# Optimization experiments

Hardware: AMD Instinct MI355X
Metric: run time of the kernel (lower is better)

The kernel has to match this reference:

```python
import jax, jax.numpy as jnp
import numpy as np

def setup_inputs() -> dict:
    key = jax.random.key(0)
    k1, k2, k3 = jax.random.split(key, 3)
    N, C, H, W = 16, 128, 128, 128
    out_chn = 128
    x = jax.random.normal(k1, (N, C, H, W), dtype=jnp.float32)
    # 1x1 conv = per-pixel linear: weight (out_chn, in_chn), bias (out_chn,)
    fan_in = C  # kernel_size=1 -> fan_in = in_chn
    bound = 1.0 / np.sqrt(fan_in)
    conv_w = jax.random.uniform(k2, (out_chn, C), dtype=jnp.float32, minval=-bound, maxval=bound)
    conv_b = jax.random.uniform(k3, (out_chn,), dtype=jnp.float32, minval=-bound, maxval=bound)
    return {"x": x, "conv_w": conv_w, "conv_b": conv_b}

def reference(x, conv_w, conv_b):
    N, C, H, W = x.shape
    x_hw = x.reshape(N, C, H * W)                     # (N, C, HW)
    logits = jnp.einsum('ncl,ndl->ncd', x_hw, x_hw)    # (N, C, C), unscaled
    weights = jax.nn.softmax(logits, axis=-1)
    attn = jnp.einsum('ncd,ndl->ncl', weights, x_hw)   # (N, C, HW)
    attn = attn.reshape(N, C, H, W)
    # 1x1 conv: contract over channel dim
    out = jnp.einsum('nchw,oc->nohw', attn, conv_w) + conv_b[None, :, None, None]
    return out
```

## Files before the change

### kernel.cpp

```cpp
#include <hip/hip_runtime.h>
#include <hip/hip_bf16.h>
#include <stdint.h>

#define NB    16
#define CD    128
#define HW    16384
#define KSPLIT 32

typedef float  f32x4  __attribute__((ext_vector_type(4)));
typedef short  bf16x8 __attribute__((ext_vector_type(8)));

__device__ __forceinline__ unsigned f2bf(float f) {
    unsigned u = __float_as_uint(f);
    u += 0x7FFFu + ((u >> 16) & 1u);
    return u >> 16;
}

__device__ __forceinline__ unsigned pk2bf(float a, float b) {
    return f2bf(a) | (f2bf(b) << 16);
}

__global__ __launch_bounds__(256, 2) void gram_kernel(const float* __restrict__ x,
                                                      float* __restrict__ P) {
    const int n  = blockIdx.x;
    const int kc = blockIdx.y;
    const int t    = threadIdx.x;
    const int wv   = t >> 6;
    const int lane = t & 63;
    const int q    = lane >> 4;
    const int r16  = lane & 15;

    __shared__ __align__(16) unsigned short Xl[CD * 132];

    f32x4 acc[4][4];
#pragma unroll
    for (int i = 0; i < 4; ++i)
#pragma unroll
        for (int j = 0; j < 4; ++j) acc[i][j] = (f32x4)0.0f;

    const int rt0 = 4 * (wv >> 1);
    const int ct0 = 4 * (wv & 1);

    const float* xb = x + (size_t)n * CD * HW;

    const int cS = t >> 5;
    const int lS = (t & 31) * 4;

    float4 stg[16];
#pragma unroll
    for (int i = 0; i < 16; ++i)
        stg[i] = *(const float4*)(xb + (size_t)(i * 8 + cS) * HW + kc * 512 + lS);

    for (int sub = 0; sub < 4; ++sub) {
#pragma unroll
        for (int i = 0; i < 16; ++i) {
            uint2 pk;
            pk.x = pk2bf(stg[i].x, stg[i].y);
            pk.y = pk2bf(stg[i].z, stg[i].w);
            *(uint2*)(&Xl[(i * 8 + cS) * 132 + lS]) = pk;
        }
        __syncthreads();

        if (sub < 3) {
            const int kb = kc * 512 + (sub + 1) * 128;
#pragma unroll
            for (int i = 0; i < 16; ++i)
                stg[i] = *(const float4*)(xb + (size_t)(i * 8 + cS) * HW + kb + lS);
        }

#pragma unroll
        for (int ks = 0; ks < 4; ++ks) {
            const int k0 = ks * 32 + q * 8;
            bf16x8 af[4], bfr[4];
#pragma unroll
            for (int i = 0; i < 4; ++i) {
                const unsigned short* pa = &Xl[(16 * (rt0 + i) + r16) * 132 + k0];
                union { bf16x8 v; uint2 u[2]; } ua;
                ua.u[0] = *(const uint2*)pa;
                ua.u[1] = *(const uint2*)(pa + 4);
                af[i] = ua.v;
                const unsigned short* pb = &Xl[(16 * (ct0 + i) + r16) * 132 + k0];
                union { bf16x8 v; uint2 u[2]; } ub;
                ub.u[0] = *(const uint2*)pb;
                ub.u[1] = *(const uint2*)(pb + 4);
                bfr[i] = ub.v;
            }
#pragma unroll
            for (int i = 0; i < 4; ++i)
#pragma unroll
                for (int j = 0; j < 4; ++j)
                    acc[i][j] = __builtin_amdgcn_mfma_f32_16x16x32_bf16(
                        af[i], bfr[j], acc[i][j], 0, 0, 0);
        }
        __syncthreads();
    }

    float* Pn = P + ((size_t)kc * NB + n) * CD * CD;
#pragma unroll
    for (int i = 0; i < 4; ++i)
#pragma unroll
        for (int j = 0; j < 4; ++j)
#pragma unroll
            for (int rr = 0; rr < 4; ++rr) {
                int row = 16 * (rt0 + i) + q * 4 + rr;
                int col = 16 * (ct0 + j) + r16;
                Pn[row * CD + col] = acc[i][j][rr];
            }
}

__global__ __launch_bounds__(256) void reduce_kernel(const float* __restrict__ P,
                                                     float* __restrict__ E) {
    const int R    = blockIdx.x * 4 + (threadIdx.x >> 6);
    const int lane = threadIdx.x & 63;
    const int n    = R >> 7;
    const int row  = R & 127;

    const float* p = P + (size_t)n * CD * CD + (size_t)row * CD;
    float s0 = 0.0f, s1 = 0.0f;
#pragma unroll
    for (int kc = 0; kc < KSPLIT; ++kc) {
        const float* pk = p + (size_t)kc * NB * CD * CD;
        s0 += pk[lane];
        s1 += pk[lane + 64];
    }
    float m = fmaxf(s0, s1);
#pragma unroll
    for (int off = 32; off > 0; off >>= 1) m = fmaxf(m, __shfl_xor(m, off));
    const float e0 = __expf(s0 - m);
    const float e1 = __expf(s1 - m);
    float e = e0 + e1;
#pragma unroll
    for (int off = 32; off > 0; off >>= 1) e += __shfl_xor(e, off);
    const float inv = 1.0f / e;

    float* g = E + (size_t)n * CD * CD + (size_t)row * CD;
    g[lane]      = e0 * inv;
    g[lane + 64] = e1 * inv;
}

__global__ __launch_bounds__(256) void mmat_kernel(const float* __restrict__ E,
                                                   const float* __restrict__ cw,
                                                   unsigned short* __restrict__ Mbf) {
    const int n  = blockIdx.x;
    const int bo = blockIdx.y;
    const int t  = threadIdx.x;
    const int o  = bo * 8 + (t >> 5);
    const int d0 = (t & 31) * 4;

    const float* En  = E + (size_t)n * CD * CD;
    const float* cwo = cw + (size_t)o * CD;

    float a0 = 0, a1 = 0, a2 = 0, a3 = 0;
#pragma unroll 8
    for (int c = 0; c < CD; ++c) {
        const float cv = cwo[c];
        float4 w = *(const float4*)&En[c * CD + d0];
        a0 += cv * w.x; a1 += cv * w.y; a2 += cv * w.z; a3 += cv * w.w;
    }
    uint2 pk;
    pk.x = pk2bf(a0, a1);
    pk.y = pk2bf(a2, a3);
    *(uint2*)&Mbf[((size_t)n * CD + o) * CD + d0] = pk;
}

__global__ __launch_bounds__(256) void out_kernel(const float* __restrict__ x,
                                                  const unsigned short* __restrict__ Mbf,
                                                  const float* __restrict__ bias,
                                                  float* __restrict__ out) {
    const int lb = blockIdx.x;
    const int n  = blockIdx.y;
    const int l0 = lb * 128;
    const int t    = threadIdx.x;
    const int wv   = t >> 6;
    const int lane = t & 63;
    const int q    = lane >> 4;
    const int r16  = lane & 15;

    __shared__ __align__(16) unsigned short Xt[128 * 128];
    __shared__ float bl[CD];

    const int lt0 = 4 * (wv >> 1);
    const int ot0 = 4 * (wv & 1);

    if (t < CD) bl[t] = bias[t];

    const float* xb = x + (size_t)n * CD * HW + l0;
    const int lt = t & 31;
    const int dg = t >> 5;
#pragma unroll
    for (int i = 0; i < 4; ++i) {
        const int d0 = i * 32 + dg * 4;
        const float* bp = xb + (size_t)d0 * HW + 4 * lt;
        float4 v0 = *(const float4*)(bp);
        float4 v1 = *(const float4*)(bp + HW);
        float4 v2 = *(const float4*)(bp + 2 * HW);
        float4 v3 = *(const float4*)(bp + 3 * HW);
        float r0[4] = {v0.x, v0.y, v0.z, v0.w};
        float r1[4] = {v1.x, v1.y, v1.z, v1.w};
        float r2[4] = {v2.x, v2.y, v2.z, v2.w};
        float r3[4] = {v3.x, v3.y, v3.z, v3.w};
        const int dph = d0 ^ (8 * (lt & 7));
#pragma unroll
        for (int j = 0; j < 4; ++j) {
            uint2 pk;
            pk.x = pk2bf(r0[j], r1[j]);
            pk.y = pk2bf(r2[j], r3[j]);
            *(uint2*)&Xt[(4 * lt + j) * 128 + dph] = pk;
        }
    }
    __syncthreads();

    f32x4 acc[4][4];
#pragma unroll
    for (int i = 0; i < 4; ++i)
#pragma unroll
        for (int j = 0; j < 4; ++j) acc[i][j] = (f32x4)0.0f;

    const unsigned short* Mn = Mbf + (size_t)n * CD * CD;
#pragma unroll
    for (int ks = 0; ks < 4; ++ks) {
        const int k0 = ks * 32 + q * 8;
        bf16x8 bfr[4];
#pragma unroll
        for (int j = 0; j < 4; ++j) {
            const int o = 16 * (ot0 + j) + r16;
            union { bf16x8 v; uint4 u; } ub;
            ub.u = *(const uint4*)&Mn[o * CD + k0];
            bfr[j] = ub.v;
        }
        bf16x8 af[4];
#pragma unroll
        for (int i = 0; i < 4; ++i) {
            const int l = 16 * (lt0 + i) + r16;
            const int doff = k0 ^ (8 * ((l >> 2) & 7));
            union { bf16x8 v; uint4 u; } ua;
            ua.u = *(const uint4*)&Xt[l * 128 + doff];
            af[i] = ua.v;
        }
#pragma unroll
        for (int i = 0; i < 4; ++i)
#pragma unroll
            for (int j = 0; j < 4; ++j)
                acc[i][j] = __builtin_amdgcn_mfma_f32_16x16x32_bf16(
                    af[i], bfr[j], acc[i][j], 0, 0, 0);
    }

    float* ob = out + (size_t)n * CD * HW + l0;
#pragma unroll
    for (int i = 0; i < 4; ++i)
#pragma unroll
        for (int j = 0; j < 4; ++j) {
            const int o = 16 * (ot0 + j) + r16;
            const int l = 16 * (lt0 + i) + q * 4;
            const float b = bl[o];
            float4 st;
            st.x = acc[i][j][0] + b;
            st.y = acc[i][j][1] + b;
            st.z = acc[i][j][2] + b;
            st.w = acc[i][j][3] + b;
            *(float4*)(ob + (size_t)o * HW + l) = st;
        }
}

extern "C" void kernel_launch(void* const* d_in, const int* in_sizes, int n_in,
                              void* d_out, int out_size, void* d_ws, size_t ws_size,
                              hipStream_t stream) {
    const float* x  = (const float*)d_in[0];
    const float* cw = (const float*)d_in[1];
    const float* cb = (const float*)d_in[2];
    float* out = (float*)d_out;

    char* ws = (char*)d_ws;
    float*          P   = (float*)(ws);
    float*          E   = (float*)(ws + (32u << 20));
    unsigned short* Mbf = (unsigned short*)(ws + (33u << 20));

    gram_kernel   <<<dim3(NB, KSPLIT), 256, 0, stream>>>(x, P);
    reduce_kernel <<<dim3(512),        256, 0, stream>>>(P, E);
    mmat_kernel   <<<dim3(NB, 16),     256, 0, stream>>>(E, cw, Mbf);
    out_kernel    <<<dim3(128, NB),    256, 0, stream>>>(x, Mbf, cb, out);
}
```

Baseline: 303.4 us.

## Fuse four stages into one cooperative kernel with grid syncs

Replaces the four separate launches (gram, reduce/softmax, weight-mix matrix, output GEMM) with a single cooperative kernel of 512 blocks that separates the stages with grid-wide syncs, keeping the separate launches as a fallback. The aim is to remove launch gaps and per-kernel tail effects between dependent stages. The reduce step also switches to float2 loads and stores. The costs are three grid barriers and a fixed 512-block grid for the output stage, where each block now loops over 4 tiles instead of one tile per block. The fused kernel needs 512 blocks to be co-resident, otherwise the cooperative launch fails and the old path runs.

Result: slower. 634.0 us (+109.0%).

```diff
diff --git a/kernel.cpp b/kernel.cpp
--- a/kernel.cpp
+++ b/kernel.cpp
@@ -1,6 +1,8 @@
 #include <hip/hip_runtime.h>
-#include <hip/hip_bf16.h>
+#include <hip/hip_cooperative_groups.h>
 #include <stdint.h>
+
+namespace cg = cooperative_groups;
 
 #define NB    16
 #define CD    128
@@ -15,9 +17,241 @@
     u += 0x7FFFu + ((u >> 16) & 1u);
     return u >> 16;
 }
-
 __device__ __forceinline__ unsigned pk2bf(float a, float b) {
     return f2bf(a) | (f2bf(b) << 16);
+}
+
+__global__ __launch_bounds__(256, 2) void fused_kernel(
+    const float* __restrict__ x, const float* __restrict__ cw,
+    const float* __restrict__ cb, float* __restrict__ P,
+    float* __restrict__ E, unsigned short* __restrict__ Mbf,
+    float* __restrict__ out)
+{
+    const int b    = blockIdx.x;
+    const int t    = threadIdx.x;
+    const int wv   = t >> 6;
+    const int lane = t & 63;
+    const int q    = lane >> 4;
+    const int r16  = lane & 15;
+
+    __shared__ __align__(16) unsigned short sh[CD * 132];
+    float* bl = (float*)(sh + CD * 128);
+
+    {
+        const int n  = b >> 5;
+        const int kc = b & 31;
+        unsigned short* Xl = sh;
+
+        f32x4 acc[4][4];
+#pragma unroll
+        for (int i = 0; i < 4; ++i)
+#pragma unroll
+            for (int j = 0; j < 4; ++j) acc[i][j] = (f32x4)0.0f;
+
+        const int rt0 = 4 * (wv >> 1);
+        const int ct0 = 4 * (wv & 1);
+        const float* xb = x + (size_t)n * CD * HW;
+        const int cS = t >> 5;
+        const int lS = (t & 31) * 4;
+
+        float4 stg[16];
+#pragma unroll
+        for (int i = 0; i < 16; ++i)
+            stg[i] = *(const float4*)(xb + (size_t)(i * 8 + cS) * HW + kc * 512 + lS);
+
+        for (int sub = 0; sub < 4; ++sub) {
+#pragma unroll
+            for (int i = 0; i < 16; ++i) {
+                uint2 pk;
+                pk.x = pk2bf(stg[i].x, stg[i].y);
+                pk.y = pk2bf(stg[i].z, stg[i].w);
+                *(uint2*)(&Xl[(i * 8 + cS) * 132 + lS]) = pk;
+            }
+            __syncthreads();
+
+            if (sub < 3) {
+                const int kb = kc * 512 + (sub + 1) * 128;
+#pragma unroll
+                for (int i = 0; i < 16; ++i)
+                    stg[i] = *(const float4*)(xb + (size_t)(i * 8 + cS) * HW + kb + lS);
+            }
+
+#pragma unroll
+            for (int ks = 0; ks < 4; ++ks) {
+                const int k0 = ks * 32 + q * 8;
+                bf16x8 af[4], bfr[4];
+#pragma unroll
+                for (int i = 0; i < 4; ++i) {
+                    const unsigned short* pa = &Xl[(16 * (rt0 + i) + r16) * 132 + k0];
+                    union { bf16x8 v; uint2 u[2]; } ua;
+                    ua.u[0] = *(const uint2*)pa;
+                    ua.u[1] = *(const uint2*)(pa + 4);
+                    af[i] = ua.v;
+                    const unsigned short* pb = &Xl[(16 * (ct0 + i) + r16) * 132 + k0];
+                    union { bf16x8 v; uint2 u[2]; } ub;
+                    ub.u[0] = *(const uint2*)pb;
+                    ub.u[1] = *(const uint2*)(pb + 4);
+                    bfr[i] = ub.v;
+                }
+#pragma unroll
+                for (int i = 0; i < 4; ++i)
+#pragma unroll
+                    for (int j = 0; j < 4; ++j)
+                        acc[i][j] = __builtin_amdgcn_mfma_f32_16x16x32_bf16(
+                            af[i], bfr[j], acc[i][j], 0, 0, 0);
+            }
+            __syncthreads();
+        }
+
+        float* Pn = P + ((size_t)kc * NB + n) * CD * CD;
+#pragma unroll
+        for (int i = 0; i < 4; ++i)
+#pragma unroll
+            for (int j = 0; j < 4; ++j)
+#pragma unroll
+                for (int rr = 0; rr < 4; ++rr) {
+                    int row = 16 * (rt0 + i) + q * 4 + rr;
+                    int col = 16 * (ct0 + j) + r16;
+                    Pn[row * CD + col] = acc[i][j][rr];
+                }
+    }
+    __threadfence();
+    cg::this_grid().sync();
+
+    {
+        const int R   = b * 4 + wv;
+        const int n2  = R >> 7;
+        const int row = R & 127;
+        const float* p = P + (size_t)n2 * CD * CD + (size_t)row * CD + 2 * lane;
+        float s0 = 0.0f, s1 = 0.0f;
+#pragma unroll
+        for (int kc = 0; kc < KSPLIT; ++kc) {
+            const float2 v = *(const float2*)(p + (size_t)kc * NB * CD * CD);
+            s0 += v.x; s1 += v.y;
+        }
+        float m = fmaxf(s0, s1);
+#pragma unroll
+        for (int off = 32; off > 0; off >>= 1) m = fmaxf(m, __shfl_xor(m, off));
+        const float e0 = __expf(s0 - m);
+        const float e1 = __expf(s1 - m);
+        float e = e0 + e1;
+#pragma unroll
+        for (int off = 32; off > 0; off >>= 1) e += __shfl_xor(e, off);
+        const float inv = 1.0f / e;
+        float2 st; st.x = e0 * inv; st.y = e1 * inv;
+        *(float2*)(E + (size_t)n2 * CD * CD + (size_t)row * CD + 2 * lane) = st;
+    }
+    __threadfence();
+    cg::this_grid().sync();
+
+    {
+        const int n3 = b >> 5;
+        const int o  = (b & 31) * 4 + wv;
+        const int d0 = 2 * lane;
+        const float* En  = E + (size_t)n3 * CD * CD + d0;
+        const float* cwo = cw + (size_t)o * CD;
+        float a0 = 0.0f, a1 = 0.0f;
+#pragma unroll 8
+        for (int c = 0; c < CD; ++c) {
+            const float cv = cwo[c];
+            const float2 w = *(const float2*)(En + c * CD);
+            a0 += cv * w.x; a1 += cv * w.y;
+        }
+        *(unsigned*)&Mbf[((size_t)n3 * CD + o) * CD + d0] = pk2bf(a0, a1);
+    }
+    __threadfence();
+    cg::this_grid().sync();
+
+    {
+        unsigned short* Xt = sh;
+        if (t < CD) bl[t] = cb[t];
+
+        const int n4 = b >> 5;
+        const int lt0 = 4 * (wv >> 1);
+        const int ot0 = 4 * (wv & 1);
+        const int lt = t & 31;
+        const int dg = t >> 5;
+        const unsigned short* Mn = Mbf + (size_t)n4 * CD * CD;
+
+        for (int r = 0; r < 4; ++r) {
+            const int l0 = ((b & 31) * 4 + r) * 128;
+            __syncthreads();
+
+            const float* xb = x + (size_t)n4 * CD * HW + l0;
+#pragma unroll
+            for (int i = 0; i < 4; ++i) {
+                const int d0 = i * 32 + dg * 4;
+                const float* bp = xb + (size_t)d0 * HW + 4 * lt;
+                float4 v0 = *(const float4*)(bp);
+                float4 v1 = *(const float4*)(bp + HW);
+                float4 v2 = *(const float4*)(bp + 2 * HW);
+                float4 v3 = *(const float4*)(bp + 3 * HW);
+                float r0[4] = {v0.x, v0.y, v0.z, v0.w};
+                float r1[4] = {v1.x, v1.y, v1.z, v1.w};
+                float r2[4] = {v2.x, v2.y, v2.z, v2.w};
+                float r3[4] = {v3.x, v3.y, v3.z, v3.w};
+                const int dph = d0 ^ (8 * (lt & 7));
+#pragma unroll
+                for (int j = 0; j < 4; ++j) {
+                    uint2 pk;
+                    pk.x = pk2bf(r0[j], r1[j]);
+                    pk.y = pk2bf(r2[j], r3[j]);
+                    *(uint2*)&Xt[(4 * lt + j) * 128 + dph] = pk;
+                }
+            }
+            __syncthreads();
+
+            f32x4 acc[4][4];
+#pragma unroll
+            for (int i = 0; i < 4; ++i)
+#pragma unroll
+                for (int j = 0; j < 4; ++j) acc[i][j] = (f32x4)0.0f;
+
+#pragma unroll
+            for (int ks = 0; ks < 4; ++ks) {
+                const int k0 = ks * 32 + q * 8;
+                bf16x8 bfr[4];
+#pragma unroll
+                for (int j = 0; j < 4; ++j) {
+                    const int o = 16 * (ot0 + j) + r16;
+                    union { bf16x8 v; uint4 u; } ub;
+                    ub.u = *(const uint4*)&Mn[o * CD + k0];
+                    bfr[j] = ub.v;
+                }
+                bf16x8 af[4];
+#pragma unroll
+                for (int i = 0; i < 4; ++i) {
+                    const int l = 16 * (lt0 + i) + r16;
+                    const int doff = k0 ^ (8 * ((l >> 2) & 7));
+                    union { bf16x8 v; uint4 u; } ua;
+                    ua.u = *(const uint4*)&Xt[l * 128 + doff];
+                    af[i] = ua.v;
+                }
+#pragma unroll
+                for (int i = 0; i < 4; ++i)
+#pragma unroll
+                    for (int j = 0; j < 4; ++j)
+                        acc[i][j] = __builtin_amdgcn_mfma_f32_16x16x32_bf16(
+                            af[i], bfr[j], acc[i][j], 0, 0, 0);
+            }
+
+            float* ob = out + (size_t)n4 * CD * HW + l0;
+#pragma unroll
+            for (int i = 0; i < 4; ++i)
+#pragma unroll
+                for (int j = 0; j < 4; ++j) {
+                    const int o = 16 * (ot0 + j) + r16;
+                    const int l = 16 * (lt0 + i) + q * 4;
+                    const float bb = bl[o];
+                    float4 st;
+                    st.x = acc[i][j][0] + bb;
+                    st.y = acc[i][j][1] + bb;
+                    st.z = acc[i][j][2] + bb;
+                    st.w = acc[i][j][3] + bb;
+                    *(float4*)(ob + (size_t)o * HW + l) = st;
+                }
+        }
+    }
 }
 
 __global__ __launch_bounds__(256, 2) void gram_kernel(const float* __restrict__ x,
@@ -40,9 +274,7 @@
 
     const int rt0 = 4 * (wv >> 1);
     const int ct0 = 4 * (wv & 1);
-
     const float* xb = x + (size_t)n * CD * HW;
-
     const int cS = t >> 5;
     const int lS = (t & 31) * 4;
 
@@ -60,14 +292,12 @@
             *(uint2*)(&Xl[(i * 8 + cS) * 132 + lS]) = pk;
         }
         __syncthreads();
-
         if (sub < 3) {
             const int kb = kc * 512 + (sub + 1) * 128;
 #pragma unroll
             for (int i = 0; i < 16; ++i)
                 stg[i] = *(const float4*)(xb + (size_t)(i * 8 + cS) * HW + kb + lS);
         }
-
 #pragma unroll
         for (int ks = 0; ks < 4; ++ks) {
             const int k0 = ks * 32 + q * 8;
@@ -115,13 +345,12 @@
     const int n    = R >> 7;
     const int row  = R & 127;
 
-    const float* p = P + (size_t)n * CD * CD + (size_t)row * CD;
+    const float* p = P + (size_t)n * CD * CD + (size_t)row * CD + 2 * lane;
     float s0 = 0.0f, s1 = 0.0f;
 #pragma unroll
     for (int kc = 0; kc < KSPLIT; ++kc) {
-        const float* pk = p + (size_t)kc * NB * CD * CD;
-        s0 += pk[lane];
-        s1 += pk[lane + 64];
+        const float2 v = *(const float2*)(p + (size_t)kc * NB * CD * CD);
+        s0 += v.x; s1 += v.y;
     }
     float m = fmaxf(s0, s1);
 #pragma unroll
@@ -132,10 +361,8 @@
 #pragma unroll
     for (int off = 32; off > 0; off >>= 1) e += __shfl_xor(e, off);
     const float inv = 1.0f / e;
-
-    float* g = E + (size_t)n * CD * CD + (size_t)row * CD;
-    g[lane]      = e0 * inv;
-    g[lane + 64] = e1 * inv;
+    float2 st; st.x = e0 * inv; st.y = e1 * inv;
+    *(float2*)(E + (size_t)n * CD * CD + (size_t)row * CD + 2 * lane) = st;
 }
 
 __global__ __launch_bounds__(256) void mmat_kernel(const float* __restrict__ E,
@@ -252,12 +479,12 @@
         for (int j = 0; j < 4; ++j) {
             const int o = 16 * (ot0 + j) + r16;
             const int l = 16 * (lt0 + i) + q * 4;
-            const float b = bl[o];
+            const float bb = bl[o];
             float4 st;
-            st.x = acc[i][j][0] + b;
-            st.y = acc[i][j][1] + b;
-            st.z = acc[i][j][2] + b;
-            st.w = acc[i][j][3] + b;
+            st.x = acc[i][j][0] + bb;
+            st.y = acc[i][j][1] + bb;
+            st.z = acc[i][j][2] + bb;
+            st.w = acc[i][j][3] + bb;
             *(float4*)(ob + (size_t)o * HW + l) = st;
         }
 }
@@ -275,8 +502,14 @@
     float*          E   = (float*)(ws + (32u << 20));
     unsigned short* Mbf = (unsigned short*)(ws + (33u << 20));
 
-    gram_kernel   <<<dim3(NB, KSPLIT), 256, 0, stream>>>(x, P);
-    reduce_kernel <<<dim3(512),        256, 0, stream>>>(P, E);
-    mmat_kernel   <<<dim3(NB, 16),     256, 0, stream>>>(E, cw, Mbf);
-    out_kernel    <<<dim3(128, NB),    256, 0, stream>>>(x, Mbf, cb, out);
-}
+    void* args[] = {(void*)&x, (void*)&cw, (void*)&cb, (void*)&P,
+                    (void*)&E, (void*)&Mbf, (void*)&out};
+    hipError_t err = hipLaunchCooperativeKernel(fused_kernel, dim3(512), dim3(256),
+                                                args, 0, stream);
+    if (err != hipSuccess) {
+        gram_kernel   <<<dim3(NB, KSPLIT), 256, 0, stream>>>(x, P);
+        reduce_kernel <<<dim3(512),        256, 0, stream>>>(P, E);
+        mmat_kernel   <<<dim3(NB, 16),     256, 0, stream>>>(E, cw, Mbf);
+        out_kernel    <<<dim3(128, NB),    256, 0, stream>>>(x, Mbf, cb, out);
+    }
+}
```

## Double-buffer gram LDS tile with XOR swizzle and vectorize reduce loads

Applied to the files above, without the earlier changes.

The gram kernel now keeps two LDS buffers. The next sub-tile is converted to bf16 and stored after the MFMA work on the current one, which removes one __syncthreads per iteration. Padding is replaced by an XOR swizzle, so fragment reads become single 16-byte LDS loads without bank conflicts. The reduce kernel reads and writes float2 per lane instead of two strided scalars. The cost is double the shared memory, which may limit occupancy at 2 blocks per CU.

New measurement: 300.8 us. About the same (-0.9%).

```diff
diff --git a/kernel.cpp b/kernel.cpp
--- a/kernel.cpp
+++ b/kernel.cpp
@@ -1,5 +1,4 @@
 #include <hip/hip_runtime.h>
-#include <hip/hip_bf16.h>
 #include <stdint.h>
 
 #define NB    16
@@ -15,7 +14,6 @@
     u += 0x7FFFu + ((u >> 16) & 1u);
     return u >> 16;
 }
-
 __device__ __forceinline__ unsigned pk2bf(float a, float b) {
     return f2bf(a) | (f2bf(b) << 16);
 }
@@ -30,7 +28,7 @@
     const int q    = lane >> 4;
     const int r16  = lane & 15;
 
-    __shared__ __align__(16) unsigned short Xl[CD * 132];
+    __shared__ __align__(16) unsigned short Xl[2 * CD * 128];
 
     f32x4 acc[4][4];
 #pragma unroll
@@ -43,46 +41,44 @@
 
     const float* xb = x + (size_t)n * CD * HW;
 
-    const int cS = t >> 5;
-    const int lS = (t & 31) * 4;
+    const int cS  = t >> 5;
+    const int lS  = (t & 31) * 4;
+    const int wsw = lS ^ (8 * cS);
+    const int rx  = 8 * (r16 & 7);
 
     float4 stg[16];
 #pragma unroll
     for (int i = 0; i < 16; ++i)
         stg[i] = *(const float4*)(xb + (size_t)(i * 8 + cS) * HW + kc * 512 + lS);
+#pragma unroll
+    for (int i = 0; i < 16; ++i) {
+        uint2 pk;
+        pk.x = pk2bf(stg[i].x, stg[i].y);
+        pk.y = pk2bf(stg[i].z, stg[i].w);
+        *(uint2*)(&Xl[(i * 8 + cS) * 128 + wsw]) = pk;
+    }
 
     for (int sub = 0; sub < 4; ++sub) {
-#pragma unroll
-        for (int i = 0; i < 16; ++i) {
-            uint2 pk;
-            pk.x = pk2bf(stg[i].x, stg[i].y);
-            pk.y = pk2bf(stg[i].z, stg[i].w);
-            *(uint2*)(&Xl[(i * 8 + cS) * 132 + lS]) = pk;
-        }
-        __syncthreads();
-
         if (sub < 3) {
             const int kb = kc * 512 + (sub + 1) * 128;
 #pragma unroll
             for (int i = 0; i < 16; ++i)
                 stg[i] = *(const float4*)(xb + (size_t)(i * 8 + cS) * HW + kb + lS);
         }
-
+        __syncthreads();
+
+        const unsigned short* Xc = &Xl[(size_t)(sub & 1) * CD * 128];
 #pragma unroll
         for (int ks = 0; ks < 4; ++ks) {
-            const int k0 = ks * 32 + q * 8;
+            const int ko = (ks * 32 + q * 8) ^ rx;
             bf16x8 af[4], bfr[4];
 #pragma unroll
             for (int i = 0; i < 4; ++i) {
-                const unsigned short* pa = &Xl[(16 * (rt0 + i) + r16) * 132 + k0];
-                union { bf16x8 v; uint2 u[2]; } ua;
-                ua.u[0] = *(const uint2*)pa;
-                ua.u[1] = *(const uint2*)(pa + 4);
+                union { bf16x8 v; uint4 u; } ua;
+                ua.u = *(const uint4*)&Xc[(16 * (rt0 + i) + r16) * 128 + ko];
                 af[i] = ua.v;
-                const unsigned short* pb = &Xl[(16 * (ct0 + i) + r16) * 132 + k0];
-                union { bf16x8 v; uint2 u[2]; } ub;
-                ub.u[0] = *(const uint2*)pb;
-                ub.u[1] = *(const uint2*)(pb + 4);
+                union { bf16x8 v; uint4 u; } ub;
+                ub.u = *(const uint4*)&Xc[(16 * (ct0 + i) + r16) * 128 + ko];
                 bfr[i] = ub.v;
             }
 #pragma unroll
@@ -92,7 +88,17 @@
                     acc[i][j] = __builtin_amdgcn_mfma_f32_16x16x32_bf16(
                         af[i], bfr[j], acc[i][j], 0, 0, 0);
         }
-        __syncthreads();
+
+        if (sub < 3) {
+            unsigned short* Xn = &Xl[(size_t)((sub + 1) & 1) * CD * 128];
+#pragma unroll
+            for (int i = 0; i < 16; ++i) {
+                uint2 pk;
+                pk.x = pk2bf(stg[i].x, stg[i].y);
+                pk.y = pk2bf(stg[i].z, stg[i].w);
+                *(uint2*)(&Xn[(i * 8 + cS) * 128 + wsw]) = pk;
+            }
+        }
     }
 
     float* Pn = P + ((size_t)kc * NB + n) * CD * CD;
@@ -115,13 +121,12 @@
     const int n    = R >> 7;
     const int row  = R & 127;
 
-    const float* p = P + (size_t)n * CD * CD + (size_t)row * CD;
+    const float* p = P + (size_t)n * CD * CD + (size_t)row * CD + 2 * lane;
     float s0 = 0.0f, s1 = 0.0f;
 #pragma unroll
     for (int kc = 0; kc < KSPLIT; ++kc) {
-        const float* pk = p + (size_t)kc * NB * CD * CD;
-        s0 += pk[lane];
-        s1 += pk[lane + 64];
+        const float2 v = *(const float2*)(p + (size_t)kc * NB * CD * CD);
+        s0 += v.x; s1 += v.y;
     }
     float m = fmaxf(s0, s1);
 #pragma unroll
@@ -132,10 +137,8 @@
 #pragma unroll
     for (int off = 32; off > 0; off >>= 1) e += __shfl_xor(e, off);
     const float inv = 1.0f / e;
-
-    float* g = E + (size_t)n * CD * CD + (size_t)row * CD;
-    g[lane]      = e0 * inv;
-    g[lane + 64] = e1 * inv;
+    float2 st; st.x = e0 * inv; st.y = e1 * inv;
+    *(float2*)(E + (size_t)n * CD * CD + (size_t)row * CD + 2 * lane) = st;
 }
 
 __global__ __launch_bounds__(256) void mmat_kernel(const float* __restrict__ E,
```
